# Kernel optimization log

Hardware: AMD Instinct MI355X
Metric: run time of the kernel (lower is better)

## Reference

```python
import jax, jax.numpy as jnp
import numpy as np

D_MODEL = 1024
NUM_HEADS = 16
D_K = D_MODEL // NUM_HEADS


def setup_inputs() -> dict:
    key = jax.random.key(0)
    ks = jax.random.split(key, 11)
    B, S = 2, 2048
    scale = 1.0 / np.sqrt(D_MODEL)
    inp = {
        'Q': jax.random.normal(ks[0], (B, S, D_MODEL), dtype=jnp.float32),
        'K': jax.random.normal(ks[1], (B, S, D_MODEL), dtype=jnp.float32),
        'V': jax.random.normal(ks[2], (B, S, D_MODEL), dtype=jnp.float32),
        'Wq': jax.random.normal(ks[3], (D_MODEL, D_MODEL), dtype=jnp.float32) * scale,
        'bq': jax.random.normal(ks[4], (D_MODEL,), dtype=jnp.float32) * scale,
        'Wk': jax.random.normal(ks[5], (D_MODEL, D_MODEL), dtype=jnp.float32) * scale,
        'bk': jax.random.normal(ks[6], (D_MODEL,), dtype=jnp.float32) * scale,
        'Wv': jax.random.normal(ks[7], (D_MODEL, D_MODEL), dtype=jnp.float32) * scale,
        'bv': jax.random.normal(ks[8], (D_MODEL,), dtype=jnp.float32) * scale,
        'Wo': jax.random.normal(ks[9], (D_MODEL, D_MODEL), dtype=jnp.float32) * scale,
        'bo': jax.random.normal(ks[10], (D_MODEL,), dtype=jnp.float32) * scale,
    }
    return inp


def _split_heads(x):
    B, S, _ = x.shape
    return x.reshape(B, S, NUM_HEADS, D_K).transpose(0, 2, 1, 3)  # [B,H,S,dk]


def reference(Q, K, V, Wq, bq, Wk, bk, Wv, bv, Wo, bo):
    # Linear projections (torch Linear: x @ W.T + b)
    q = _split_heads(Q @ Wq.T + bq)
    k = _split_heads(K @ Wk.T + bk)
    v = _split_heads(V @ Wv.T + bv)
    scores = jnp.einsum('bhqd,bhkd->bhqk', q, k) / jnp.sqrt(jnp.float32(D_K))
    probs = jax.nn.softmax(scores, axis=-1)
    out = jnp.einsum('bhqk,bhkd->bhqd', probs, v)  # [B,H,S,dk]
    B, H, S, dk = out.shape
    out = out.transpose(0, 2, 1, 3).reshape(B, S, D_MODEL)
    return out @ Wo.T + bo
```

## Files before the change

kernel.cpp:

```cpp
#include <hip/hip_runtime.h>
#include <hip/hip_bf16.h>

#define DEV __device__ __forceinline__

#define BATCH 2
#define SEQ   2048
#define DMODEL 1024
#define NHEAD 16
#define DK    64
#define MROWS (BATCH*SEQ)
#define KD    1024
#define GEMM_NT (KD/32)

typedef __attribute__((ext_vector_type(4))) float f32x4;
typedef __attribute__((ext_vector_type(8))) short s16x8;
typedef __attribute__((ext_vector_type(4))) short s16x4;
typedef __attribute__((ext_vector_type(4))) float fvec4;

__device__ short g_X[3][MROWS*DMODEL];
__device__ short g_W[4][DMODEL*DMODEL];
__device__ short g_q [MROWS*DMODEL];
__device__ short g_k [MROWS*DMODEL];
__device__ short g_vt[MROWS*DMODEL];
__device__ short g_at[MROWS*DMODEL];

DEV short f2bf(float f) {
  union { __hip_bfloat16 h; short s; } u;
  u.h = __float2bfloat16(f);
  return u.s;
}

DEV void gload_lds16(const void* g, void* l) {
  __builtin_amdgcn_global_load_lds(
      (const __attribute__((address_space(1))) void*)g,
      (__attribute__((address_space(3))) void*)l, 16, 0, 0);
}

__global__ __launch_bounds__(256) void cast3(const float* __restrict__ a,
                                             const float* __restrict__ b,
                                             const float* __restrict__ c, int n8) {
  const float* src = blockIdx.z == 0 ? a : blockIdx.z == 1 ? b : c;
  short* dst = g_X[blockIdx.z];
  int i = blockIdx.x * 256 + threadIdx.x;
  if (i < n8) {
    const fvec4* p = (const fvec4*)(src + (size_t)i*8);
    fvec4 v0 = p[0], v1 = p[1];
    s16x8 r;
    r[0]=f2bf(v0[0]); r[1]=f2bf(v0[1]); r[2]=f2bf(v0[2]); r[3]=f2bf(v0[3]);
    r[4]=f2bf(v1[0]); r[5]=f2bf(v1[1]); r[6]=f2bf(v1[2]); r[7]=f2bf(v1[3]);
    *(s16x8*)(dst + (size_t)i*8) = r;
  }
}

__global__ __launch_bounds__(256) void cast4(const float* __restrict__ a,
                                             const float* __restrict__ b,
                                             const float* __restrict__ c,
                                             const float* __restrict__ d, int n8) {
  const float* src = blockIdx.z == 0 ? a : blockIdx.z == 1 ? b
                   : blockIdx.z == 2 ? c : d;
  short* dst = g_W[blockIdx.z];
  int i = blockIdx.x * 256 + threadIdx.x;
  if (i < n8) {
    const fvec4* p = (const fvec4*)(src + (size_t)i*8);
    fvec4 v0 = p[0], v1 = p[1];
    s16x8 r;
    r[0]=f2bf(v0[0]); r[1]=f2bf(v0[1]); r[2]=f2bf(v0[2]); r[3]=f2bf(v0[3]);
    r[4]=f2bf(v1[0]); r[5]=f2bf(v1[1]); r[6]=f2bf(v1[2]); r[7]=f2bf(v1[3]);
    *(s16x8*)(dst + (size_t)i*8) = r;
  }
}

struct GemmSmem { short As[3][128*32]; short Bs[3][128*32]; };

DEV void gemm_core(GemmSmem& sm, const short* __restrict__ A,
                   const short* __restrict__ Bw, const float* __restrict__ bias,
                   void* __restrict__ outp, float scale, int mode,
                   int rowBase, int colBase) {
  const int t = threadIdx.x, l = t & 63, w = t >> 6, g = l >> 4;
  const int wr = w >> 1, wc = w & 1;

  f32x4 acc[4][4] = {};

  auto stage = [&](int buf, int k0) {
#pragma unroll
    for (int j = 0; j < 2; ++j) {
      int e = w*1024 + j*512 + l*8;
      int e2 = e ^ (((e >> 7) & 3) << 3);
      int r = e2 >> 5, c = e2 & 31;
      gload_lds16(A  + (size_t)(rowBase + r)*KD + k0 + c, &sm.As[buf][w*1024 + j*512]);
      gload_lds16(Bw + (size_t)(colBase + r)*KD + k0 + c, &sm.Bs[buf][w*1024 + j*512]);
    }
  };

  stage(0, 0);
  stage(1, 32);

  int cur = 0, nxt = 2;
  for (int i = 0; i < GEMM_NT; ++i) {
    if (i < GEMM_NT - 1) asm volatile("s_waitcnt vmcnt(4)" ::: "memory");
    else                 asm volatile("s_waitcnt vmcnt(0)" ::: "memory");
    __builtin_amdgcn_s_barrier();
    __builtin_amdgcn_sched_barrier(0);

    s16x8 a[4], b[4];
#pragma unroll
    for (int x = 0; x < 4; ++x) {
      int ra = wr*64 + x*16 + (l & 15);
      int ia = (ra*32 + g*8) ^ (((ra >> 2) & 3) << 3);
      a[x] = *(const s16x8*)&sm.As[cur][ia];
      int rb = wc*64 + x*16 + (l & 15);
      int ib = (rb*32 + g*8) ^ (((rb >> 2) & 3) << 3);
      b[x] = *(const s16x8*)&sm.Bs[cur][ib];
    }
    if (i + 2 < GEMM_NT) stage(nxt, (i + 2)*32);
    __builtin_amdgcn_sched_barrier(0);

    __builtin_amdgcn_s_setprio(1);
#pragma unroll
    for (int x = 0; x < 4; ++x)
#pragma unroll
      for (int jn = 0; jn < 4; ++jn)
        acc[x][jn] = __builtin_amdgcn_mfma_f32_16x16x32_bf16(a[x], b[jn], acc[x][jn], 0, 0, 0);
    __builtin_amdgcn_s_setprio(0);

    cur = cur == 2 ? 0 : cur + 1;
    nxt = nxt == 2 ? 0 : nxt + 1;
  }

#pragma unroll
  for (int x = 0; x < 4; ++x) {
    int mrow0 = rowBase + wr*64 + x*16 + g*4;
#pragma unroll
    for (int jn = 0; jn < 4; ++jn) {
      int n = colBase + wc*64 + jn*16 + (l & 15);
      float bv = bias[n];
#pragma unroll
      for (int r = 0; r < 4; ++r) {
        int m = mrow0 + r;
        float val = (acc[x][jn][r] + bv) * scale;
        if (mode == 1) {
          int b = m >> 11, s = m & 2047, h = n >> 6, d = n & 63;
          ((short*)outp)[(((size_t)(b*NHEAD + h)*SEQ + s)*DK) + d] = f2bf(val);
        } else if (mode == 2) {
          int b = m >> 11, s = m & 2047, h = n >> 6, d = n & 63;
          ((short*)outp)[((size_t)(b*NHEAD + h)*DK + d)*SEQ + s] = f2bf(val);
        } else {
          ((float*)outp)[(size_t)m*DMODEL + n] = val;
        }
      }
    }
  }
}

__global__ __launch_bounds__(256, 3)
void proj_qkv(const float* __restrict__ bq, const float* __restrict__ bk,
              const float* __restrict__ bv) {
  __shared__ GemmSmem sm;
  int z = blockIdx.z;
  int orig = blockIdx.y*8 + blockIdx.x;
  int swz = (orig & 7)*32 + (orig >> 3);
  int bx = swz & 7, by = swz >> 3;
  const float* bias = z == 0 ? bq : z == 1 ? bk : bv;
  void* outp = z == 0 ? (void*)g_q : z == 1 ? (void*)g_k : (void*)g_vt;
  gemm_core(sm, g_X[z], g_W[z], bias, outp, z == 0 ? 0.125f : 1.0f,
            z == 2 ? 2 : 1, by*128, bx*128);
}

__global__ __launch_bounds__(256, 3)
void proj_out(const float* __restrict__ bo, float* __restrict__ out) {
  __shared__ GemmSmem sm;
  int orig = blockIdx.y*8 + blockIdx.x;
  int swz = (orig & 7)*32 + (orig >> 3);
  int bx = swz & 7, by = swz >> 3;
  gemm_core(sm, g_at, g_W[3], bo, out, 1.0f, 3, by*128, bx*128);
}

__global__ __launch_bounds__(256, 4)
void attn_kernel(short* __restrict__ aout) {
  __shared__ short qs[64*64];
  __shared__ short ks[2][64*64];
  __shared__ short vs[2][64*64];

  const int t = threadIdx.x, l = t & 63, w = t >> 6, g = l >> 4;
  const int q15 = l & 15;
  int orig = blockIdx.y*32 + blockIdx.x;
  int swz = (orig & 7)*128 + (orig >> 3);
  const int qblk = swz & 31, bh = swz >> 5;
  const int qbase = qblk * 64;
  const size_t hoff = (size_t)bh * SEQ * DK;

  auto stage_kv = [&](int buf, int kt) {
#pragma unroll
    for (int j = 0; j < 2; ++j) {
      int e = w*1024 + j*512 + l*8;
      int e2 = e ^ (((e >> 6) & 7) << 3);
      gload_lds16(g_k + hoff + (size_t)kt*DK + e2, &ks[buf][w*1024 + j*512]);
      gload_lds16(g_vt + hoff + (size_t)(e2 >> 6)*SEQ + kt + (e2 & 63),
                  &vs[buf][w*1024 + j*512]);
    }
  };

  {
#pragma unroll
    for (int j = 0; j < 2; ++j) {
      int e = w*1024 + j*512 + l*8;
      int e2 = e ^ (((e >> 6) & 7) << 3);
      gload_lds16(g_q + hoff + (size_t)qbase*DK + e2, &qs[w*1024 + j*512]);
    }
    stage_kv(0, 0);
  }
  __syncthreads();

  s16x8 qf[2];
#pragma unroll
  for (int kf = 0; kf < 2; ++kf) {
    int row = w*16 + q15;
    int idx = (row*64 + kf*32 + g*8) ^ ((row & 7) << 3);
    qf[kf] = *(const s16x8*)&qs[idx];
  }

  float mrun = -1e30f, lrun = 0.f;
  f32x4 o[4] = {};

  int cur = 0;
  for (int kt = 0; kt < SEQ; kt += 64) {
    if (kt + 64 < SEQ) stage_kv(cur ^ 1, kt + 64);

    f32x4 sc[4] = {};
    __builtin_amdgcn_s_setprio(1);
#pragma unroll
    for (int ni = 0; ni < 4; ++ni)
#pragma unroll
      for (int kf = 0; kf < 2; ++kf) {
        int row = ni*16 + q15;
        int idx = (row*64 + kf*32 + g*8) ^ ((row & 7) << 3);
        s16x8 afr = *(const s16x8*)&ks[cur][idx];
        sc[ni] = __builtin_amdgcn_mfma_f32_16x16x32_bf16(afr, qf[kf], sc[ni], 0, 0, 0);
      }
    __builtin_amdgcn_s_setprio(0);

    float m0 = fmaxf(fmaxf(sc[0][0], sc[0][1]), fmaxf(sc[0][2], sc[0][3]));
    float m1 = fmaxf(fmaxf(sc[1][0], sc[1][1]), fmaxf(sc[1][2], sc[1][3]));
    float m2 = fmaxf(fmaxf(sc[2][0], sc[2][1]), fmaxf(sc[2][2], sc[2][3]));
    float m3 = fmaxf(fmaxf(sc[3][0], sc[3][1]), fmaxf(sc[3][2], sc[3][3]));
    float mt = fmaxf(fmaxf(m0, m1), fmaxf(m2, m3));
    mt = fmaxf(mt, __shfl_xor(mt, 16));
    mt = fmaxf(mt, __shfl_xor(mt, 32));

    bool need_rescale = __any(mt > mrun + 8.0f);
    float mnew = need_rescale ? fmaxf(mrun, mt) : mrun;

    float p[4][4];
#pragma unroll
    for (int ni = 0; ni < 4; ++ni)
#pragma unroll
      for (int r = 0; r < 4; ++r)
        p[ni][r] = __expf(sc[ni][r] - mnew);

    float s0 = (p[0][0]+p[0][1]) + (p[0][2]+p[0][3]);
    float s1 = (p[1][0]+p[1][1]) + (p[1][2]+p[1][3]);
    float s2 = (p[2][0]+p[2][1]) + (p[2][2]+p[2][3]);
    float s3 = (p[3][0]+p[3][1]) + (p[3][2]+p[3][3]);
    float s = (s0+s1) + (s2+s3);
    s += __shfl_xor(s, 16);
    s += __shfl_xor(s, 32);

#pragma unroll
    for (int ni = 0; ni < 4; ++ni) {
      s16x4 pv;
#pragma unroll
      for (int r = 0; r < 4; ++r) pv[r] = f2bf(p[ni][r]);
      int idx = w*1024 + q15*64 + ((ni*16 + g*4) ^ ((q15 & 7) << 3));
      *(s16x4*)&qs[idx] = pv;
    }

    if (need_rescale) {
      float alpha = __expf(mrun - mnew);
      lrun = lrun * alpha + s;
      mrun = mnew;
      float av[4];
#pragma unroll
      for (int r = 0; r < 4; ++r)
        av[r] = __shfl(alpha, (l & 48) | (g*4 + r));
#pragma unroll
      for (int nd = 0; nd < 4; ++nd)
#pragma unroll
        for (int r = 0; r < 4; ++r)
          o[nd][r] *= av[r];
    } else {
      lrun += s;
    }

    asm volatile("s_waitcnt lgkmcnt(0)" ::: "memory");
    __builtin_amdgcn_sched_barrier(0);

    s16x8 pa[2];
#pragma unroll
    for (int kf = 0; kf < 2; ++kf) {
      int idx = w*1024 + q15*64 + ((kf*32 + g*8) ^ ((q15 & 7) << 3));
      pa[kf] = *(const s16x8*)&qs[idx];
    }

    __builtin_amdgcn_s_setprio(1);
#pragma unroll
    for (int nd = 0; nd < 4; ++nd)
#pragma unroll
      for (int kf = 0; kf < 2; ++kf) {
        int row = nd*16 + q15;
        int idx = (row*64 + kf*32 + g*8) ^ ((row & 7) << 3);
        s16x8 bfr = *(const s16x8*)&vs[cur][idx];
        o[nd] = __builtin_amdgcn_mfma_f32_16x16x32_bf16(pa[kf], bfr, o[nd], 0, 0, 0);
      }
    __builtin_amdgcn_s_setprio(0);

    asm volatile("s_waitcnt vmcnt(0)" ::: "memory");
    __builtin_amdgcn_s_barrier();
    __builtin_amdgcn_sched_barrier(0);
    cur ^= 1;
  }

  float inv = 1.0f / lrun;
  float iv[4];
#pragma unroll
  for (int r = 0; r < 4; ++r)
    iv[r] = __shfl(inv, (l & 48) | (g*4 + r));

  int b = bh >> 4, h = bh & 15;
#pragma unroll
  for (int nd = 0; nd < 4; ++nd) {
    int dcol = h*DK + nd*16 + q15;
#pragma unroll
    for (int r = 0; r < 4; ++r) {
      int srow = qbase + w*16 + g*4 + r;
      aout[((size_t)(b*SEQ + srow))*DMODEL + dcol] = f2bf(o[nd][r] * iv[r]);
    }
  }
}

extern "C" void kernel_launch(void* const* d_in, const int* in_sizes, int n_in,
                              void* d_out, int out_size, void* d_ws, size_t ws_size,
                              hipStream_t stream) {
  const float* Q  = (const float*)d_in[0];
  const float* K  = (const float*)d_in[1];
  const float* V  = (const float*)d_in[2];
  const float* Wq = (const float*)d_in[3];
  const float* bq = (const float*)d_in[4];
  const float* Wk = (const float*)d_in[5];
  const float* bk = (const float*)d_in[6];
  const float* Wv = (const float*)d_in[7];
  const float* bv = (const float*)d_in[8];
  const float* Wo = (const float*)d_in[9];
  const float* bo = (const float*)d_in[10];

  short* pat;
  hipGetSymbolAddress((void**)&pat, HIP_SYMBOL(g_at));

  const int nX8 = MROWS*DMODEL/8;
  const int nW8 = DMODEL*DMODEL/8;
  dim3 blk(256);

  cast3<<<dim3(nX8/256, 1, 3), blk, 0, stream>>>(Q, K, V, nX8);
  cast4<<<dim3(nW8/256, 1, 4), blk, 0, stream>>>(Wq, Wk, Wv, Wo, nW8);
  proj_qkv<<<dim3(DMODEL/128, MROWS/128, 3), blk, 0, stream>>>(bq, bk, bv);
  attn_kernel<<<dim3(SEQ/64, BATCH*NHEAD), blk, 0, stream>>>(pat);
  proj_out<<<dim3(DMODEL/128, MROWS/128), blk, 0, stream>>>(bo, (float*)d_out);
}
```

Before: 152.7 us.

## Process two query row groups per wave in attention with 128-thread blocks

Attention blocks shrink from four waves to two, and each wave now handles 32 query rows as two 16-row groups. Each K and V fragment read from LDS feeds two MFMAs, which halves LDS fragment traffic per unit of compute. Softmax state, P staging and output writes are duplicated per group. In exchange the kernel uses more registers per wave, has fewer waves per block to hide latency, and the launch bound changes to 128 threads with 2 blocks.

```diff
diff --git a/kernel.cpp b/kernel.cpp
--- a/kernel.cpp
+++ b/kernel.cpp
@@ -175,7 +175,7 @@
   gemm_core(sm, g_at, g_W[3], bo, out, 1.0f, 3, by*128, bx*128);
 }
 
-__global__ __launch_bounds__(256, 4)
+__global__ __launch_bounds__(128, 2)
 void attn_kernel(short* __restrict__ aout) {
   __shared__ short qs[64*64];
   __shared__ short ks[2][64*64];
@@ -191,42 +191,44 @@
 
   auto stage_kv = [&](int buf, int kt) {
 #pragma unroll
-    for (int j = 0; j < 2; ++j) {
-      int e = w*1024 + j*512 + l*8;
+    for (int j = 0; j < 4; ++j) {
+      int e = j*1024 + w*512 + l*8;
       int e2 = e ^ (((e >> 6) & 7) << 3);
-      gload_lds16(g_k + hoff + (size_t)kt*DK + e2, &ks[buf][w*1024 + j*512]);
+      gload_lds16(g_k + hoff + (size_t)kt*DK + e2, &ks[buf][j*1024 + w*512]);
       gload_lds16(g_vt + hoff + (size_t)(e2 >> 6)*SEQ + kt + (e2 & 63),
-                  &vs[buf][w*1024 + j*512]);
+                  &vs[buf][j*1024 + w*512]);
     }
   };
 
   {
 #pragma unroll
-    for (int j = 0; j < 2; ++j) {
-      int e = w*1024 + j*512 + l*8;
+    for (int j = 0; j < 4; ++j) {
+      int e = j*1024 + w*512 + l*8;
       int e2 = e ^ (((e >> 6) & 7) << 3);
-      gload_lds16(g_q + hoff + (size_t)qbase*DK + e2, &qs[w*1024 + j*512]);
+      gload_lds16(g_q + hoff + (size_t)qbase*DK + e2, &qs[j*1024 + w*512]);
     }
     stage_kv(0, 0);
   }
   __syncthreads();
 
-  s16x8 qf[2];
-#pragma unroll
-  for (int kf = 0; kf < 2; ++kf) {
-    int row = w*16 + q15;
-    int idx = (row*64 + kf*32 + g*8) ^ ((row & 7) << 3);
-    qf[kf] = *(const s16x8*)&qs[idx];
-  }
-
-  float mrun = -1e30f, lrun = 0.f;
-  f32x4 o[4] = {};
+  s16x8 qf[2][2];
+#pragma unroll
+  for (int grp = 0; grp < 2; ++grp)
+#pragma unroll
+    for (int kf = 0; kf < 2; ++kf) {
+      int row = w*32 + grp*16 + q15;
+      int idx = (row*64 + kf*32 + g*8) ^ ((row & 7) << 3);
+      qf[grp][kf] = *(const s16x8*)&qs[idx];
+    }
+
+  float mrun[2] = {-1e30f, -1e30f}, lrun[2] = {0.f, 0.f};
+  f32x4 o[2][4] = {};
 
   int cur = 0;
   for (int kt = 0; kt < SEQ; kt += 64) {
     if (kt + 64 < SEQ) stage_kv(cur ^ 1, kt + 64);
 
-    f32x4 sc[4] = {};
+    f32x4 sc[2][4] = {};
     __builtin_amdgcn_s_setprio(1);
 #pragma unroll
     for (int ni = 0; ni < 4; ++ni)
@@ -235,71 +237,88 @@
         int row = ni*16 + q15;
         int idx = (row*64 + kf*32 + g*8) ^ ((row & 7) << 3);
         s16x8 afr = *(const s16x8*)&ks[cur][idx];
-        sc[ni] = __builtin_amdgcn_mfma_f32_16x16x32_bf16(afr, qf[kf], sc[ni], 0, 0, 0);
+        sc[0][ni] = __builtin_amdgcn_mfma_f32_16x16x32_bf16(afr, qf[0][kf], sc[0][ni], 0, 0, 0);
+        sc[1][ni] = __builtin_amdgcn_mfma_f32_16x16x32_bf16(afr, qf[1][kf], sc[1][ni], 0, 0, 0);
       }
     __builtin_amdgcn_s_setprio(0);
 
-    float m0 = fmaxf(fmaxf(sc[0][0], sc[0][1]), fmaxf(sc[0][2], sc[0][3]));
-    float m1 = fmaxf(fmaxf(sc[1][0], sc[1][1]), fmaxf(sc[1][2], sc[1][3]));
-    float m2 = fmaxf(fmaxf(sc[2][0], sc[2][1]), fmaxf(sc[2][2], sc[2][3]));
-    float m3 = fmaxf(fmaxf(sc[3][0], sc[3][1]), fmaxf(sc[3][2], sc[3][3]));
-    float mt = fmaxf(fmaxf(m0, m1), fmaxf(m2, m3));
-    mt = fmaxf(mt, __shfl_xor(mt, 16));
-    mt = fmaxf(mt, __shfl_xor(mt, 32));
-
-    bool need_rescale = __any(mt > mrun + 8.0f);
-    float mnew = need_rescale ? fmaxf(mrun, mt) : mrun;
-
-    float p[4][4];
-#pragma unroll
-    for (int ni = 0; ni < 4; ++ni)
-#pragma unroll
-      for (int r = 0; r < 4; ++r)
-        p[ni][r] = __expf(sc[ni][r] - mnew);
-
-    float s0 = (p[0][0]+p[0][1]) + (p[0][2]+p[0][3]);
-    float s1 = (p[1][0]+p[1][1]) + (p[1][2]+p[1][3]);
-    float s2 = (p[2][0]+p[2][1]) + (p[2][2]+p[2][3]);
-    float s3 = (p[3][0]+p[3][1]) + (p[3][2]+p[3][3]);
-    float s = (s0+s1) + (s2+s3);
-    s += __shfl_xor(s, 16);
-    s += __shfl_xor(s, 32);
-
-#pragma unroll
-    for (int ni = 0; ni < 4; ++ni) {
-      s16x4 pv;
-#pragma unroll
-      for (int r = 0; r < 4; ++r) pv[r] = f2bf(p[ni][r]);
-      int idx = w*1024 + q15*64 + ((ni*16 + g*4) ^ ((q15 & 7) << 3));
-      *(s16x4*)&qs[idx] = pv;
-    }
+    float p[2][4][4];
+    float s[2], mt[2];
+#pragma unroll
+    for (int grp = 0; grp < 2; ++grp) {
+      float m0 = fmaxf(fmaxf(sc[grp][0][0], sc[grp][0][1]), fmaxf(sc[grp][0][2], sc[grp][0][3]));
+      float m1 = fmaxf(fmaxf(sc[grp][1][0], sc[grp][1][1]), fmaxf(sc[grp][1][2], sc[grp][1][3]));
+      float m2 = fmaxf(fmaxf(sc[grp][2][0], sc[grp][2][1]), fmaxf(sc[grp][2][2], sc[grp][2][3]));
+      float m3 = fmaxf(fmaxf(sc[grp][3][0], sc[grp][3][1]), fmaxf(sc[grp][3][2], sc[grp][3][3]));
+      float m = fmaxf(fmaxf(m0, m1), fmaxf(m2, m3));
+      m = fmaxf(m, __shfl_xor(m, 16));
+      m = fmaxf(m, __shfl_xor(m, 32));
+      mt[grp] = m;
+    }
+
+    bool need_rescale = __any((mt[0] > mrun[0] + 8.0f) || (mt[1] > mrun[1] + 8.0f));
+    float mnew[2];
+#pragma unroll
+    for (int grp = 0; grp < 2; ++grp) {
+      mnew[grp] = need_rescale ? fmaxf(mrun[grp], mt[grp]) : mrun[grp];
+#pragma unroll
+      for (int ni = 0; ni < 4; ++ni)
+#pragma unroll
+        for (int r = 0; r < 4; ++r)
+          p[grp][ni][r] = __expf(sc[grp][ni][r] - mnew[grp]);
+      float s0 = (p[grp][0][0]+p[grp][0][1]) + (p[grp][0][2]+p[grp][0][3]);
+      float s1 = (p[grp][1][0]+p[grp][1][1]) + (p[grp][1][2]+p[grp][1][3]);
+      float s2 = (p[grp][2][0]+p[grp][2][1]) + (p[grp][2][2]+p[grp][2][3]);
+      float s3 = (p[grp][3][0]+p[grp][3][1]) + (p[grp][3][2]+p[grp][3][3]);
+      float ss = (s0+s1) + (s2+s3);
+      ss += __shfl_xor(ss, 16);
+      ss += __shfl_xor(ss, 32);
+      s[grp] = ss;
+    }
+
+#pragma unroll
+    for (int grp = 0; grp < 2; ++grp)
+#pragma unroll
+      for (int ni = 0; ni < 4; ++ni) {
+        s16x4 pv;
+#pragma unroll
+        for (int r = 0; r < 4; ++r) pv[r] = f2bf(p[grp][ni][r]);
+        int idx = w*2048 + grp*1024 + q15*64 + ((ni*16 + g*4) ^ ((q15 & 7) << 3));
+        *(s16x4*)&qs[idx] = pv;
+      }
 
     if (need_rescale) {
-      float alpha = __expf(mrun - mnew);
-      lrun = lrun * alpha + s;
-      mrun = mnew;
-      float av[4];
-#pragma unroll
-      for (int r = 0; r < 4; ++r)
-        av[r] = __shfl(alpha, (l & 48) | (g*4 + r));
-#pragma unroll
-      for (int nd = 0; nd < 4; ++nd)
+#pragma unroll
+      for (int grp = 0; grp < 2; ++grp) {
+        float alpha = __expf(mrun[grp] - mnew[grp]);
+        lrun[grp] = lrun[grp] * alpha + s[grp];
+        mrun[grp] = mnew[grp];
+        float av[4];
 #pragma unroll
         for (int r = 0; r < 4; ++r)
-          o[nd][r] *= av[r];
+          av[r] = __shfl(alpha, (l & 48) | (g*4 + r));
+#pragma unroll
+        for (int nd = 0; nd < 4; ++nd)
+#pragma unroll
+          for (int r = 0; r < 4; ++r)
+            o[grp][nd][r] *= av[r];
+      }
     } else {
-      lrun += s;
+      lrun[0] += s[0];
+      lrun[1] += s[1];
     }
 
     asm volatile("s_waitcnt lgkmcnt(0)" ::: "memory");
     __builtin_amdgcn_sched_barrier(0);
 
-    s16x8 pa[2];
-#pragma unroll
-    for (int kf = 0; kf < 2; ++kf) {
-      int idx = w*1024 + q15*64 + ((kf*32 + g*8) ^ ((q15 & 7) << 3));
-      pa[kf] = *(const s16x8*)&qs[idx];
-    }
+    s16x8 pa[2][2];
+#pragma unroll
+    for (int grp = 0; grp < 2; ++grp)
+#pragma unroll
+      for (int kf = 0; kf < 2; ++kf) {
+        int idx = w*2048 + grp*1024 + q15*64 + ((kf*32 + g*8) ^ ((q15 & 7) << 3));
+        pa[grp][kf] = *(const s16x8*)&qs[idx];
+      }
 
     __builtin_amdgcn_s_setprio(1);
 #pragma unroll
@@ -309,7 +328,8 @@
         int row = nd*16 + q15;
         int idx = (row*64 + kf*32 + g*8) ^ ((row & 7) << 3);
         s16x8 bfr = *(const s16x8*)&vs[cur][idx];
-        o[nd] = __builtin_amdgcn_mfma_f32_16x16x32_bf16(pa[kf], bfr, o[nd], 0, 0, 0);
+        o[0][nd] = __builtin_amdgcn_mfma_f32_16x16x32_bf16(pa[0][kf], bfr, o[0][nd], 0, 0, 0);
+        o[1][nd] = __builtin_amdgcn_mfma_f32_16x16x32_bf16(pa[1][kf], bfr, o[1][nd], 0, 0, 0);
       }
     __builtin_amdgcn_s_setprio(0);
 
@@ -319,20 +339,22 @@
     cur ^= 1;
   }
 
-  float inv = 1.0f / lrun;
-  float iv[4];
-#pragma unroll
-  for (int r = 0; r < 4; ++r)
-    iv[r] = __shfl(inv, (l & 48) | (g*4 + r));
-
   int b = bh >> 4, h = bh & 15;
 #pragma unroll
-  for (int nd = 0; nd < 4; ++nd) {
-    int dcol = h*DK + nd*16 + q15;
-#pragma unroll
-    for (int r = 0; r < 4; ++r) {
-      int srow = qbase + w*16 + g*4 + r;
-      aout[((size_t)(b*SEQ + srow))*DMODEL + dcol] = f2bf(o[nd][r] * iv[r]);
+  for (int grp = 0; grp < 2; ++grp) {
+    float inv = 1.0f / lrun[grp];
+    float iv[4];
+#pragma unroll
+    for (int r = 0; r < 4; ++r)
+      iv[r] = __shfl(inv, (l & 48) | (g*4 + r));
+#pragma unroll
+    for (int nd = 0; nd < 4; ++nd) {
+      int dcol = h*DK + nd*16 + q15;
+#pragma unroll
+      for (int r = 0; r < 4; ++r) {
+        int srow = qbase + w*32 + grp*16 + g*4 + r;
+        aout[((size_t)(b*SEQ + srow))*DMODEL + dcol] = f2bf(o[grp][nd][r] * iv[r]);
+      }
     }
   }
 }
@@ -362,6 +384,6 @@
   cast3<<<dim3(nX8/256, 1, 3), blk, 0, stream>>>(Q, K, V, nX8);
   cast4<<<dim3(nW8/256, 1, 4), blk, 0, stream>>>(Wq, Wk, Wv, Wo, nW8);
   proj_qkv<<<dim3(DMODEL/128, MROWS/128, 3), blk, 0, stream>>>(bq, bk, bv);
-  attn_kernel<<<dim3(SEQ/64, BATCH*NHEAD), blk, 0, stream>>>(pat);
+  attn_kernel<<<dim3(SEQ/64, BATCH*NHEAD), dim3(128), 0, stream>>>(pat);
   proj_out<<<dim3(DMODEL/128, MROWS/128), blk, 0, stream>>>(bo, (float*)d_out);
 }
```

After: 160.7 us. 1.05x slower.
